# Optimization experiments

Measured on AMD Instinct MI355X. Metric: run time of the kernel, lower is better.

Reference implementation:

```python
import jax, jax.numpy as jnp
import numpy as np

B, T, S, PD = 512, 2048, 16, 4

def setup_inputs() -> dict:
    key = jax.random.key(0)
    ks = jax.random.split(key, 10)
    w = lambda k, sh: (jax.random.normal(k, sh, dtype=jnp.float32) * 0.1)
    return {
        'z': jax.random.normal(ks[0], (B, T, S), dtype=jnp.float32),
        'p': jax.random.normal(ks[1], (B, T, PD), dtype=jnp.float32),
        'mu0': jnp.zeros((B, S), dtype=jnp.float32),
        'P0': jnp.full((B, S), 0.1, dtype=jnp.float32),  # cfg['kf_P0']
        'Wq1': w(ks[2], (PD, 64)), 'bq1': jnp.zeros((64,), jnp.float32),
        'Wq2': w(ks[3], (64, S)),  'bq2': jnp.zeros((S,), jnp.float32),
        'Wr1': w(ks[4], (PD, 64)), 'br1': jnp.zeros((64,), jnp.float32),
        'Wr2': w(ks[5], (64, S)),  'br2': jnp.zeros((S,), jnp.float32),
        'Wg1': w(ks[6], (PD, 32)), 'bg1': jnp.zeros((32,), jnp.float32),
        'Wg2': w(ks[7], (32, 1)),  'bg2': jnp.zeros((1,), jnp.float32),
    }

def _mlp(x, W1, b1, W2, b2):
    return jax.nn.relu(x @ W1 + b1) @ W2 + b2

def reference(z, p, mu0, P0, Wq1, bq1, Wq2, bq2, Wr1, br1, Wr2, br2, Wg1, bg1, Wg2, bg2):
    # z: [B,T,S], p: [B,T,PD]; scan over time with batched Kalman state.
    zT = jnp.swapaxes(z, 0, 1)  # [T,B,S]
    pT = jnp.swapaxes(p, 0, 1)  # [T,B,PD]

    def step(carry, inp):
        mu, P = carry            # [B,S], [B,S]
        z_t, p_t = inp           # [B,S], [B,PD]
        Q_t = jax.nn.softplus(_mlp(p_t, Wq1, bq1, Wq2, bq2)) + 1e-8
        R_t = jax.nn.softplus(_mlp(p_t, Wr1, br1, Wr2, br2)) + 1e-8
        P_pred = P + Q_t
        K = jnp.clip(P_pred / (P_pred + R_t), 1e-6, 0.95)
        gamma_t = jax.nn.sigmoid(_mlp(p_t, Wg1, bg1, Wg2, bg2))  # [B,1] (scalar per sample)
        mu_new = mu + gamma_t * (K * (z_t - mu))
        P_new = (1.0 - K) * P_pred
        return (mu_new, P_new), mu_new

    (mu_f, P_f), mus = jax.lax.scan(step, (mu0, P0), (zT, pT))
    return jnp.swapaxes(mus, 0, 1)  # [B,T,S]
```

## Files before the change

kernel.cpp:

```cpp
#include <hip/hip_runtime.h>
#include <hip/hip_fp16.h>
#include <stdint.h>
#include <math.h>

#define KB 512
#define KT 2048
#define KS 16
#define KPD 4
#define QT 512
#define NQ (KT / QT)
#define QSTR 515
#define HSTR 40

typedef _Float16 f16;
typedef _Float16 f16x8 __attribute__((ext_vector_type(8)));
typedef float f32x4 __attribute__((ext_vector_type(4)));

#define MFMA16(A, B, C) __builtin_amdgcn_mfma_f32_16x16x32_f16(A, B, C, 0, 0, 0)

__device__ __forceinline__ float softplus_f(float x) {
    float ax = fabsf(x);
    float e  = __expf(-ax);
    return fmaxf(x, 0.0f) + __logf(1.0f + e);
}
__device__ __forceinline__ float sigmoid_f(float x) {
    return __builtin_amdgcn_rcpf(1.0f + __expf(-x));
}
__device__ __forceinline__ float h2f_lo(uint32_t w) {
    return __half2float(__ushort_as_half((unsigned short)(w & 0xffffu)));
}
__device__ __forceinline__ float h2f_hi(uint32_t w) {
    return __half2float(__ushort_as_half((unsigned short)(w >> 16)));
}
__device__ __forceinline__ f16x8 zero8() {
    f16x8 v;
#pragma unroll
    for (int i = 0; i < 8; ++i) v[i] = (f16)0;
    return v;
}
__device__ __forceinline__ int spos(int t) { return t ^ ((t >> 5) & 31); }

__device__ __forceinline__ uint32_t pkrelu(float a, float b) {
    auto h = __builtin_amdgcn_cvt_pkrtz(fmaxf(a, 0.f), fmaxf(b, 0.f));
    uint32_t w; __builtin_memcpy(&w, &h, 4);
    return w;
}
__device__ __forceinline__ uint16_t f2h(float x) {
    return (uint16_t)__half_as_ushort(__float2half_rn(x));
}
__device__ __forceinline__ float h2f(uint16_t x) {
    return __half2float(__ushort_as_half((unsigned short)x));
}

__global__ __launch_bounds__(512, 2) void kalman_ilp(
    const float* __restrict__ z, const float* __restrict__ p,
    const float* __restrict__ mu0, const float* __restrict__ P0,
    const float* __restrict__ Wq1, const float* __restrict__ bq1,
    const float* __restrict__ Wq2, const float* __restrict__ bq2,
    const float* __restrict__ Wr1, const float* __restrict__ br1,
    const float* __restrict__ Wr2, const float* __restrict__ br2,
    const float* __restrict__ Wg1, const float* __restrict__ bg1,
    const float* __restrict__ Wg2, const float* __restrict__ bg2,
    float* __restrict__ out)
{
    __shared__ __align__(16) uint32_t QRl[KS * QSTR];
    __shared__ __align__(16) float    Gl[QT];
    __shared__ __align__(16) uint16_t Hs[8 * KS * HSTR];
    __shared__ __align__(16) uint16_t zsh[KS * QSTR];

    const int tid = threadIdx.x;
    const int wv = tid >> 6;
    const int l = tid & 63;
    const int g = l >> 4;
    const int c = l & 15;
    const int b = blockIdx.x;

    f16* __restrict__ Hw = reinterpret_cast<f16*>(Hs) + wv * (KS * HSTR);

    const float* __restrict__ zb = z + (size_t)b * KT * KS;
    const float* __restrict__ pb = p + (size_t)b * KT * KPD;
    float* __restrict__ ob = out + (size_t)b * KT * KS;

    f16x8 fA1[10];
#pragma unroll
    for (int m = 0; m < 10; ++m) {
        const float* W = (m < 4) ? (Wq1 + m * 16)
                       : (m < 8) ? (Wr1 + (m - 4) * 16)
                                 : (Wg1 + (m - 8) * 16);
        const int ld = (m < 8) ? 64 : 32;
        float w0 = W[0 * ld + c], w1 = W[1 * ld + c],
              w2 = W[2 * ld + c], w3 = W[3 * ld + c];
        f16x8 a = zero8();
        if (g == 0) { a[0] = (f16)w0; a[1] = (f16)w1; a[2] = (f16)w2; a[3] = (f16)w3; }
        fA1[m] = a;
    }
    f16x8 fA2[5];
#pragma unroll
    for (int i = 0; i < 4; ++i) {
        const float* W = (i < 2) ? Wq2 : Wr2;
        const int kb = (i & 1) * 32;
        f16x8 a;
#pragma unroll
        for (int j = 0; j < 8; ++j) a[j] = (f16)W[(kb + g * 8 + j) * 16 + c];
        fA2[i] = a;
    }
    {
        f16x8 a = zero8();
        if (c == 0) {
#pragma unroll
            for (int j = 0; j < 8; ++j) a[j] = (f16)Wg2[g * 8 + j];
        }
        fA2[4] = a;
    }
    const float bQ0 = bq2[g * 4 + 0], bQ1 = bq2[g * 4 + 1],
                bQ2 = bq2[g * 4 + 2], bQ3 = bq2[g * 4 + 3];
    const float bR0 = br2[g * 4 + 0], bR1 = br2[g * 4 + 1],
                bR2 = br2[g * 4 + 2], bR3 = br2[g * 4 + 3];
    const float bG = bg2[0];

    float muA = mu0[b * KS + wv],     PA = P0[b * KS + wv];
    float muB = mu0[b * KS + wv + 8], PB = P0[b * KS + wv + 8];

    auto scan2 = [&](int sA, int sB, float& muqA, float& PqA, float& muqB, float& PqB) {
        uint32_t qrA[8], qrB[8];
        float zvA[8], zvB[8], gv[8];
        const uint32_t* qrowA = QRl + (size_t)sA * QSTR;
        const uint32_t* qrowB = QRl + (size_t)sB * QSTR;
#pragma unroll
        for (int i = 0; i < 8; ++i) {
            const int ps = spos(l * 8 + i);
            qrA[i] = qrowA[ps];
            qrB[i] = qrowB[ps];
            zvA[i] = h2f(zsh[sA * QSTR + ps]);
            zvB[i] = h2f(zsh[sB * QSTR + ps]);
            gv[i] = Gl[ps];
        }
        float a00 = 1.f, a01 = 0.f, a10 = 0.f, a11 = 1.f;
        float b00 = 1.f, b01 = 0.f, b10 = 0.f, b11 = 1.f;
#pragma unroll
        for (int i = 0; i < 8; ++i) {
            float QA = h2f_lo(qrA[i]), RA = h2f_hi(qrA[i]);
            float QB = h2f_lo(qrB[i]), RB = h2f_hi(qrB[i]);
            float taA = fmaf(QA, a10, a00), tbA = fmaf(QA, a11, a01);
            float taB = fmaf(QB, b10, b00), tbB = fmaf(QB, b11, b01);
            float n10A = fmaf(QA + RA, a10, a00), n11A = fmaf(QA + RA, a11, a01);
            float n10B = fmaf(QB + RB, b10, b00), n11B = fmaf(QB + RB, b11, b01);
            a00 = RA * taA; a01 = RA * tbA; a10 = n10A; a11 = n11A;
            b00 = RB * taB; b01 = RB * tbB; b10 = n10B; b11 = n11B;
        }
        float rnA = __builtin_amdgcn_rcpf(a11);
        float rnB = __builtin_amdgcn_rcpf(b11);
        float maA = a00 * rnA, mbA = a01 * rnA, mcA = a10 * rnA;
        float maB = b00 * rnB, mbB = b01 * rnB, mcB = b10 * rnB;
#pragma unroll
        for (int r = 0; r < 6; ++r) {
            const int d = 1 << r;
            float paA = __shfl_up(maA, d), pbA = __shfl_up(mbA, d), pcA = __shfl_up(mcA, d);
            float paB = __shfl_up(maB, d), pbB = __shfl_up(mbB, d), pcB = __shfl_up(mcB, d);
            float naA = fmaf(maA, paA, mbA * pcA);
            float naB = fmaf(maB, paB, mbB * pcB);
            float nbA = fmaf(maA, pbA, mbA);
            float nbB = fmaf(maB, pbB, mbB);
            float ncA = fmaf(mcA, paA, pcA);
            float ncB = fmaf(mcB, paB, pcB);
            float ndA = fmaf(mcA, pbA, 1.f);
            float ndB = fmaf(mcB, pbB, 1.f);
            float rrA = __builtin_amdgcn_rcpf(ndA);
            float rrB = __builtin_amdgcn_rcpf(ndB);
            bool act = (l >= d);
            maA = act ? naA * rrA : maA;  mbA = act ? nbA * rrA : mbA;  mcA = act ? ncA * rrA : mcA;
            maB = act ? naB * rrB : maB;  mbB = act ? nbB * rrB : mbB;  mcB = act ? ncB * rrB : mcB;
        }
        float eaA = __shfl_up(maA, 1), ebA = __shfl_up(mbA, 1), ecA = __shfl_up(mcA, 1);
        float eaB = __shfl_up(maB, 1), ebB = __shfl_up(mbB, 1), ecB = __shfl_up(mcB, 1);
        if (l == 0) { eaA = 1.f; ebA = 0.f; ecA = 0.f; eaB = 1.f; ebB = 0.f; ecB = 0.f; }
        float Pa = fmaf(eaA, PqA, ebA) * __builtin_amdgcn_rcpf(fmaf(ecA, PqA, 1.f));
        float Pb = fmaf(eaB, PqB, ebB) * __builtin_amdgcn_rcpf(fmaf(ecB, PqB, 1.f));

        float avA[8], bwA[8], avB[8], bwB[8];
        float AA = 1.f, BA = 0.f, AB = 1.f, BB = 0.f;
#pragma unroll
        for (int i = 0; i < 8; ++i) {
            float QA = h2f_lo(qrA[i]), RA = h2f_hi(qrA[i]);
            float QB = h2f_lo(qrB[i]), RB = h2f_hi(qrB[i]);
            float PpA = Pa + QA;
            float PpB = Pb + QB;
            float K0A = PpA * __builtin_amdgcn_rcpf(PpA + RA);
            float K0B = PpB * __builtin_amdgcn_rcpf(PpB + RB);
            float KkA = __builtin_amdgcn_fmed3f(K0A, 1e-6f, 0.95f);
            float KkB = __builtin_amdgcn_fmed3f(K0B, 1e-6f, 0.95f);
            float gkA = gv[i] * KkA;
            float gkB = gv[i] * KkB;
            avA[i] = 1.f - gkA;  bwA[i] = gkA * zvA[i];
            avB[i] = 1.f - gkB;  bwB[i] = gkB * zvB[i];
            Pa = fmaf(-KkA, PpA, PpA);
            Pb = fmaf(-KkB, PpB, PpB);
            AA = AA * avA[i];  BA = fmaf(avA[i], BA, bwA[i]);
            AB = AB * avB[i];  BB = fmaf(avB[i], BB, bwB[i]);
        }
        float PendA = __shfl(Pa, 63);
        float PendB = __shfl(Pb, 63);
#pragma unroll
        for (int r = 0; r < 6; ++r) {
            const int d = 1 << r;
            float pAA = __shfl_up(AA, d), pBA = __shfl_up(BA, d);
            float pAB = __shfl_up(AB, d), pBB = __shfl_up(BB, d);
            float nAA = AA * pAA;
            float nAB = AB * pAB;
            float nBA = fmaf(AA, pBA, BA);
            float nBB = fmaf(AB, pBB, BB);
            bool act = (l >= d);
            AA = act ? nAA : AA;  BA = act ? nBA : BA;
            AB = act ? nAB : AB;  BB = act ? nBB : BB;
        }
        float eAA = __shfl_up(AA, 1), eBA = __shfl_up(BA, 1);
        float eAB = __shfl_up(AB, 1), eBB = __shfl_up(BB, 1);
        if (l == 0) { eAA = 1.f; eBA = 0.f; eAB = 1.f; eBB = 0.f; }
        float muA_ = fmaf(eAA, muqA, eBA);
        float muB_ = fmaf(eAB, muqB, eBB);
#pragma unroll
        for (int i = 0; i < 8; ++i) {
            muA_ = fmaf(avA[i], muA_, bwA[i]);
            muB_ = fmaf(avB[i], muB_, bwB[i]);
            const int ps = spos(l * 8 + i);
            zsh[sA * QSTR + ps] = f2h(muA_);
            zsh[sB * QSTR + ps] = f2h(muB_);
        }
        muqA = __shfl(muA_, 63);
        muqB = __shfl(muB_, 63);
        PqA = PendA;
        PqB = PendB;
    };

    for (int q = 0; q < NQ; ++q) {
        {
            const int trow = q * QT + wv * 64;
            const float4 pv = *reinterpret_cast<const float4*>(pb + (size_t)(trow + l) * KPD);

#pragma unroll
            for (int n = 0; n < 4; ++n) {
                f16x8 fBP;
                {
                    const int src = n * 16 + c;
                    float x = __shfl(pv.x, src);
                    float y = __shfl(pv.y, src);
                    float zz = __shfl(pv.z, src);
                    float w = __shfl(pv.w, src);
                    fBP = zero8();
                    if (g == 0) { fBP[0] = (f16)x; fBP[1] = (f16)y; fBP[2] = (f16)zz; fBP[3] = (f16)w; }
                }

                f32x4 aq; aq[0] = bQ0; aq[1] = bQ1; aq[2] = bQ2; aq[3] = bQ3;
                f32x4 ar; ar[0] = bR0; ar[1] = bR1; ar[2] = bR2; ar[3] = bR3;
                f32x4 ag; ag[0] = 0.f; ag[1] = 0.f; ag[2] = 0.f; ag[3] = 0.f;

                uint32_t* Hd = reinterpret_cast<uint32_t*>(Hw);

#pragma unroll
                for (int X = 0; X < 5; ++X) {
                    const int m0 = 2 * X, m1 = 2 * X + 1;
                    {
                        const float* bs = (m0 < 4) ? (bq1 + m0 * 16)
                                        : (m0 < 8) ? (br1 + (m0 - 4) * 16)
                                                   : (bg1 + (m0 - 8) * 16);
                        f32x4 acc;
                        acc[0] = bs[g * 4 + 0]; acc[1] = bs[g * 4 + 1];
                        acc[2] = bs[g * 4 + 2]; acc[3] = bs[g * 4 + 3];
                        acc = MFMA16(fA1[m0], fBP, acc);
                        Hd[c * 20 + g * 2 + 0] = pkrelu(acc[0], acc[1]);
                        Hd[c * 20 + g * 2 + 1] = pkrelu(acc[2], acc[3]);
                    }
                    {
                        const float* bs = (m1 < 4) ? (bq1 + m1 * 16)
                                        : (m1 < 8) ? (br1 + (m1 - 4) * 16)
                                                   : (bg1 + (m1 - 8) * 16);
                        f32x4 acc;
                        acc[0] = bs[g * 4 + 0]; acc[1] = bs[g * 4 + 1];
                        acc[2] = bs[g * 4 + 2]; acc[3] = bs[g * 4 + 3];
                        acc = MFMA16(fA1[m1], fBP, acc);
                        Hd[c * 20 + 8 + g * 2 + 0] = pkrelu(acc[0], acc[1]);
                        Hd[c * 20 + 8 + g * 2 + 1] = pkrelu(acc[2], acc[3]);
                    }
                    f16x8 fb = *reinterpret_cast<const f16x8*>(Hw + c * HSTR + g * 8);
                    if (X == 0)      aq = MFMA16(fA2[0], fb, aq);
                    else if (X == 1) aq = MFMA16(fA2[1], fb, aq);
                    else if (X == 2) ar = MFMA16(fA2[2], fb, ar);
                    else if (X == 3) ar = MFMA16(fA2[3], fb, ar);
                    else             ag = MFMA16(fA2[4], fb, ag);
                }

                const int tt = wv * 64 + n * 16 + c;
                const int ps = spos(tt);
#pragma unroll
                for (int i = 0; i < 4; ++i) {
                    float Qv = softplus_f(aq[i]) + 1e-8f;
                    float Rv = softplus_f(ar[i]) + 1e-8f;
                    auto pk = __builtin_amdgcn_cvt_pkrtz(Qv, Rv);
                    uint32_t w; __builtin_memcpy(&w, &pk, 4);
                    QRl[(size_t)(g * 4 + i) * QSTR + ps] = w;
                }
                if (g == 0)
                    Gl[ps] = sigmoid_f(ag[0] + bG);
            }

            const float4* zq = reinterpret_cast<const float4*>(zb + (size_t)q * QT * KS);
#pragma unroll
            for (int v = 0; v < 4; ++v) {
                int k = tid + 512 * v;
                float4 w = zq[k];
                int t = k >> 2, s0 = (k & 3) << 2;
                const int ps = spos(t);
                zsh[(s0 + 0) * QSTR + ps] = f2h(w.x);
                zsh[(s0 + 1) * QSTR + ps] = f2h(w.y);
                zsh[(s0 + 2) * QSTR + ps] = f2h(w.z);
                zsh[(s0 + 3) * QSTR + ps] = f2h(w.w);
            }
        }
        __syncthreads();

        scan2(wv, wv + 8, muA, PA, muB, PB);
        __syncthreads();

        {
            float* od = ob + (size_t)q * QT * KS;
#pragma unroll
            for (int v = 0; v < 4; ++v) {
                int k = tid + 512 * v;
                int t = k >> 2, s0 = (k & 3) << 2;
                const int ps = spos(t);
                float4 w;
                w.x = h2f(zsh[(s0 + 0) * QSTR + ps]);
                w.y = h2f(zsh[(s0 + 1) * QSTR + ps]);
                w.z = h2f(zsh[(s0 + 2) * QSTR + ps]);
                w.w = h2f(zsh[(s0 + 3) * QSTR + ps]);
                *reinterpret_cast<float4*>(od + 4 * (size_t)k) = w;
            }
        }
        __syncthreads();
    }
}

__global__ __launch_bounds__(512, 2) void kalman_one(
    const float* __restrict__ z, const float* __restrict__ p,
    const float* __restrict__ mu0, const float* __restrict__ P0,
    const float* __restrict__ Wq1, const float* __restrict__ bq1,
    const float* __restrict__ Wq2, const float* __restrict__ bq2,
    const float* __restrict__ Wr1, const float* __restrict__ br1,
    const float* __restrict__ Wr2, const float* __restrict__ br2,
    const float* __restrict__ Wg1, const float* __restrict__ bg1,
    const float* __restrict__ Wg2, const float* __restrict__ bg2,
    float* __restrict__ out)
{
    __shared__ __align__(16) uint32_t QRl[KS * QSTR];
    __shared__ __align__(16) float    Gl[QT];
    __shared__ __align__(16) uint16_t Hs[8 * KS * HSTR];
    __shared__ __align__(16) uint16_t zsh[KS * QSTR];

    const int tid = threadIdx.x;
    const int wv = tid >> 6;
    const int l = tid & 63;
    const int g = l >> 4;
    const int c = l & 15;
    const int b = blockIdx.x;

    f16* __restrict__ Hw = reinterpret_cast<f16*>(Hs) + wv * (KS * HSTR);

    const float* __restrict__ zb = z + (size_t)b * KT * KS;
    const float* __restrict__ pb = p + (size_t)b * KT * KPD;
    float* __restrict__ ob = out + (size_t)b * KT * KS;

    f16x8 fA1[10];
#pragma unroll
    for (int m = 0; m < 10; ++m) {
        const float* W = (m < 4) ? (Wq1 + m * 16)
                       : (m < 8) ? (Wr1 + (m - 4) * 16)
                                 : (Wg1 + (m - 8) * 16);
        const int ld = (m < 8) ? 64 : 32;
        float w0 = W[0 * ld + c], w1 = W[1 * ld + c],
              w2 = W[2 * ld + c], w3 = W[3 * ld + c];
        f16x8 a = zero8();
        if (g == 0) { a[0] = (f16)w0; a[1] = (f16)w1; a[2] = (f16)w2; a[3] = (f16)w3; }
        fA1[m] = a;
    }
    f16x8 fA2[5];
#pragma unroll
    for (int i = 0; i < 4; ++i) {
        const float* W = (i < 2) ? Wq2 : Wr2;
        const int kb = (i & 1) * 32;
        f16x8 a;
#pragma unroll
        for (int j = 0; j < 8; ++j) a[j] = (f16)W[(kb + g * 8 + j) * 16 + c];
        fA2[i] = a;
    }
    {
        f16x8 a = zero8();
        if (c == 0) {
#pragma unroll
            for (int j = 0; j < 8; ++j) a[j] = (f16)Wg2[g * 8 + j];
        }
        fA2[4] = a;
    }
    const float bQ0 = bq2[g * 4 + 0], bQ1 = bq2[g * 4 + 1],
                bQ2 = bq2[g * 4 + 2], bQ3 = bq2[g * 4 + 3];
    const float bR0 = br2[g * 4 + 0], bR1 = br2[g * 4 + 1],
                bR2 = br2[g * 4 + 2], bR3 = br2[g * 4 + 3];
    const float bG = bg2[0];

    float muA = mu0[b * KS + wv],     PA = P0[b * KS + wv];
    float muB = mu0[b * KS + wv + 8], PB = P0[b * KS + wv + 8];

    auto scan_s = [&](int s, float& mu_q, float& P_q) {
        uint32_t qr[8];
        const uint32_t* qrow = QRl + (size_t)s * QSTR;
        float zvv[8], gvv[8];
#pragma unroll
        for (int i = 0; i < 8; ++i) {
            const int ps = spos(l * 8 + i);
            qr[i] = qrow[ps];
            zvv[i] = h2f(zsh[s * QSTR + ps]);
            gvv[i] = Gl[ps];
        }
        float c00 = 1.f, c01 = 0.f, c10 = 0.f, c11 = 1.f;
#pragma unroll
        for (int i = 0; i < 8; ++i) {
            float Q = h2f_lo(qr[i]), Rr = h2f_hi(qr[i]);
            float ta = fmaf(Q, c10, c00);
            float tb = fmaf(Q, c11, c01);
            float n10 = fmaf(Q + Rr, c10, c00);
            float n11 = fmaf(Q + Rr, c11, c01);
            c00 = Rr * ta; c01 = Rr * tb; c10 = n10; c11 = n11;
        }
        float rn = __builtin_amdgcn_rcpf(c11);
        float ma = c00 * rn, mb = c01 * rn, mc = c10 * rn;
#pragma unroll
        for (int r = 0; r < 6; ++r) {
            const int d = 1 << r;
            float pa = __shfl_up(ma, d);
            float pbv = __shfl_up(mb, d);
            float pc = __shfl_up(mc, d);
            float na = fmaf(ma, pa, mb * pc);
            float nb = fmaf(ma, pbv, mb);
            float nc = fmaf(mc, pa, pc);
            float nd = fmaf(mc, pbv, 1.f);
            float rr = __builtin_amdgcn_rcpf(nd);
            bool act = (l >= d);
            ma = act ? na * rr : ma;
            mb = act ? nb * rr : mb;
            mc = act ? nc * rr : mc;
        }
        float ea = __shfl_up(ma, 1);
        float eb = __shfl_up(mb, 1);
        float ec = __shfl_up(mc, 1);
        if (l == 0) { ea = 1.f; eb = 0.f; ec = 0.f; }
        float P = fmaf(ea, P_q, eb) * __builtin_amdgcn_rcpf(fmaf(ec, P_q, 1.f));

        float av[8], bw[8];
        float A = 1.f, Bv = 0.f;
#pragma unroll
        for (int i = 0; i < 8; ++i) {
            float Q = h2f_lo(qr[i]), Rr = h2f_hi(qr[i]);
            float Pp = P + Q;
            float K0 = Pp * __builtin_amdgcn_rcpf(Pp + Rr);
            float Kk = __builtin_amdgcn_fmed3f(K0, 1e-6f, 0.95f);
            float gk = gvv[i] * Kk;
            av[i] = 1.f - gk;
            bw[i] = gk * zvv[i];
            P = fmaf(-Kk, Pp, Pp);
            A = A * av[i];
            Bv = fmaf(av[i], Bv, bw[i]);
        }
        float P_end = __shfl(P, 63);
#pragma unroll
        for (int r = 0; r < 6; ++r) {
            const int d = 1 << r;
            float pA = __shfl_up(A, d);
            float pB = __shfl_up(Bv, d);
            float nA = A * pA;
            float nB = fmaf(A, pB, Bv);
            bool act = (l >= d);
            A  = act ? nA : A;
            Bv = act ? nB : Bv;
        }
        float eA = __shfl_up(A, 1);
        float eB = __shfl_up(Bv, 1);
        if (l == 0) { eA = 1.f; eB = 0.f; }
        float mu = fmaf(eA, mu_q, eB);
#pragma unroll
        for (int i = 0; i < 8; ++i) {
            mu = fmaf(av[i], mu, bw[i]);
            zsh[s * QSTR + spos(l * 8 + i)] = f2h(mu);
        }
        mu_q = __shfl(mu, 63);
        P_q = P_end;
    };

    for (int q = 0; q < NQ; ++q) {
        {
            const int trow = q * QT + wv * 64;
            const float4 pv = *reinterpret_cast<const float4*>(pb + (size_t)(trow + l) * KPD);

#pragma unroll
            for (int n = 0; n < 4; ++n) {
                f16x8 fBP;
                {
                    const int src = n * 16 + c;
                    float x = __shfl(pv.x, src);
                    float y = __shfl(pv.y, src);
                    float zz = __shfl(pv.z, src);
                    float w = __shfl(pv.w, src);
                    fBP = zero8();
                    if (g == 0) { fBP[0] = (f16)x; fBP[1] = (f16)y; fBP[2] = (f16)zz; fBP[3] = (f16)w; }
                }

                f32x4 aq; aq[0] = bQ0; aq[1] = bQ1; aq[2] = bQ2; aq[3] = bQ3;
                f32x4 ar; ar[0] = bR0; ar[1] = bR1; ar[2] = bR2; ar[3] = bR3;
                f32x4 ag; ag[0] = 0.f; ag[1] = 0.f; ag[2] = 0.f; ag[3] = 0.f;

                uint32_t* Hd = reinterpret_cast<uint32_t*>(Hw);

#pragma unroll
                for (int X = 0; X < 5; ++X) {
                    const int m0 = 2 * X, m1 = 2 * X + 1;
                    {
                        const float* bs = (m0 < 4) ? (bq1 + m0 * 16)
                                        : (m0 < 8) ? (br1 + (m0 - 4) * 16)
                                                   : (bg1 + (m0 - 8) * 16);
                        f32x4 acc;
                        acc[0] = bs[g * 4 + 0]; acc[1] = bs[g * 4 + 1];
                        acc[2] = bs[g * 4 + 2]; acc[3] = bs[g * 4 + 3];
                        acc = MFMA16(fA1[m0], fBP, acc);
                        Hd[c * 20 + g * 2 + 0] = pkrelu(acc[0], acc[1]);
                        Hd[c * 20 + g * 2 + 1] = pkrelu(acc[2], acc[3]);
                    }
                    {
                        const float* bs = (m1 < 4) ? (bq1 + m1 * 16)
                                        : (m1 < 8) ? (br1 + (m1 - 4) * 16)
                                                   : (bg1 + (m1 - 8) * 16);
                        f32x4 acc;
                        acc[0] = bs[g * 4 + 0]; acc[1] = bs[g * 4 + 1];
                        acc[2] = bs[g * 4 + 2]; acc[3] = bs[g * 4 + 3];
                        acc = MFMA16(fA1[m1], fBP, acc);
                        Hd[c * 20 + 8 + g * 2 + 0] = pkrelu(acc[0], acc[1]);
                        Hd[c * 20 + 8 + g * 2 + 1] = pkrelu(acc[2], acc[3]);
                    }
                    f16x8 fb = *reinterpret_cast<const f16x8*>(Hw + c * HSTR + g * 8);
                    if (X == 0)      aq = MFMA16(fA2[0], fb, aq);
                    else if (X == 1) aq = MFMA16(fA2[1], fb, aq);
                    else if (X == 2) ar = MFMA16(fA2[2], fb, ar);
                    else if (X == 3) ar = MFMA16(fA2[3], fb, ar);
                    else             ag = MFMA16(fA2[4], fb, ag);
                }

                const int tt = wv * 64 + n * 16 + c;
                const int ps = spos(tt);
#pragma unroll
                for (int i = 0; i < 4; ++i) {
                    float Qv = softplus_f(aq[i]) + 1e-8f;
                    float Rv = softplus_f(ar[i]) + 1e-8f;
                    auto pk = __builtin_amdgcn_cvt_pkrtz(Qv, Rv);
                    uint32_t w; __builtin_memcpy(&w, &pk, 4);
                    QRl[(size_t)(g * 4 + i) * QSTR + ps] = w;
                }
                if (g == 0)
                    Gl[ps] = sigmoid_f(ag[0] + bG);
            }

            const float4* zq = reinterpret_cast<const float4*>(zb + (size_t)q * QT * KS);
#pragma unroll
            for (int v = 0; v < 4; ++v) {
                int k = tid + 512 * v;
                float4 w = zq[k];
                int t = k >> 2, s0 = (k & 3) << 2;
                const int ps = spos(t);
                zsh[(s0 + 0) * QSTR + ps] = f2h(w.x);
                zsh[(s0 + 1) * QSTR + ps] = f2h(w.y);
                zsh[(s0 + 2) * QSTR + ps] = f2h(w.z);
                zsh[(s0 + 3) * QSTR + ps] = f2h(w.w);
            }
        }
        __syncthreads();

        scan_s(wv, muA, PA);
        scan_s(wv + 8, muB, PB);
        __syncthreads();

        {
            float* od = ob + (size_t)q * QT * KS;
#pragma unroll
            for (int v = 0; v < 4; ++v) {
                int k = tid + 512 * v;
                int t = k >> 2, s0 = (k & 3) << 2;
                const int ps = spos(t);
                float4 w;
                w.x = h2f(zsh[(s0 + 0) * QSTR + ps]);
                w.y = h2f(zsh[(s0 + 1) * QSTR + ps]);
                w.z = h2f(zsh[(s0 + 2) * QSTR + ps]);
                w.w = h2f(zsh[(s0 + 3) * QSTR + ps]);
                *reinterpret_cast<float4*>(od + 4 * (size_t)k) = w;
            }
        }
        __syncthreads();
    }
}

extern "C" void kernel_launch(void* const* d_in, const int* in_sizes, int n_in,
                              void* d_out, int out_size, void* d_ws, size_t ws_size,
                              hipStream_t stream) {
    const float* z   = (const float*)d_in[0];
    const float* p   = (const float*)d_in[1];
    const float* mu0 = (const float*)d_in[2];
    const float* P0  = (const float*)d_in[3];
    const float* Wq1 = (const float*)d_in[4];
    const float* bq1 = (const float*)d_in[5];
    const float* Wq2 = (const float*)d_in[6];
    const float* bq2 = (const float*)d_in[7];
    const float* Wr1 = (const float*)d_in[8];
    const float* br1 = (const float*)d_in[9];
    const float* Wr2 = (const float*)d_in[10];
    const float* br2 = (const float*)d_in[11];
    const float* Wg1 = (const float*)d_in[12];
    const float* bg1 = (const float*)d_in[13];
    const float* Wg2 = (const float*)d_in[14];
    const float* bg2 = (const float*)d_in[15];
    float* out = (float*)d_out;

    hipFuncAttributes attr{};
    bool use_ilp = false;
    if (hipFuncGetAttributes(&attr, (const void*)kalman_ilp) == hipSuccess)
        use_ilp = (attr.localSizeBytes <= 16);

    if (use_ilp) {
        hipLaunchKernelGGL(kalman_ilp, dim3(KB), dim3(512), 0, stream,
                           z, p, mu0, P0, Wq1, bq1, Wq2, bq2,
                           Wr1, br1, Wr2, br2, Wg1, bg1, Wg2, bg2, out);
    } else {
        hipLaunchKernelGGL(kalman_one, dim3(KB), dim3(512), 0, stream,
                           z, p, mu0, P0, Wq1, bq1, Wq2, bq2,
                           Wr1, br1, Wr2, br2, Wg1, bg1, Wg2, bg2, out);
    }
}
```

Baseline: 86.89 us.

## Shrink Kalman block to 256 threads with 256-step chunks and four states per wave

Replaces the 512-thread kernel with a 256-thread variant that processes time in 256-step chunks. Each wave now scans four state channels through two scan2 calls, and each lane handles 4 timesteps instead of 8. Shared memory per block shrinks, so more blocks can be resident at once. The cost is a longer serial chain per wave, twice as many chunk iterations with their syncs, and more shuffle-based prefix rounds relative to the sequential work per lane.

```diff
diff --git a/kernel.cpp b/kernel.cpp
--- a/kernel.cpp
+++ b/kernel.cpp
@@ -7,6 +7,9 @@
 #define KT 2048
 #define KS 16
 #define KPD 4
+#define ET 256
+#define NE (KT / ET)
+#define ESTR 259
 #define QT 512
 #define NQ (KT / QT)
 #define QSTR 515
@@ -52,7 +55,7 @@
     return __half2float(__ushort_as_half((unsigned short)x));
 }
 
-__global__ __launch_bounds__(512, 2) void kalman_ilp(
+__global__ __launch_bounds__(256, 2) void kalman_small(
     const float* __restrict__ z, const float* __restrict__ p,
     const float* __restrict__ mu0, const float* __restrict__ P0,
     const float* __restrict__ Wq1, const float* __restrict__ bq1,
@@ -63,10 +66,10 @@
     const float* __restrict__ Wg2, const float* __restrict__ bg2,
     float* __restrict__ out)
 {
-    __shared__ __align__(16) uint32_t QRl[KS * QSTR];
-    __shared__ __align__(16) float    Gl[QT];
-    __shared__ __align__(16) uint16_t Hs[8 * KS * HSTR];
-    __shared__ __align__(16) uint16_t zsh[KS * QSTR];
+    __shared__ __align__(16) uint32_t QRl[KS * ESTR];
+    __shared__ __align__(16) float    Gl[ET];
+    __shared__ __align__(16) uint16_t Hs[4 * KS * HSTR];
+    __shared__ __align__(16) uint16_t zsh[KS * ESTR];
 
     const int tid = threadIdx.x;
     const int wv = tid >> 6;
@@ -118,27 +121,29 @@
                 bR2 = br2[g * 4 + 2], bR3 = br2[g * 4 + 3];
     const float bG = bg2[0];
 
-    float muA = mu0[b * KS + wv],     PA = P0[b * KS + wv];
-    float muB = mu0[b * KS + wv + 8], PB = P0[b * KS + wv + 8];
+    float muA = mu0[b * KS + wv + 0],  PA = P0[b * KS + wv + 0];
+    float muB = mu0[b * KS + wv + 4],  PB = P0[b * KS + wv + 4];
+    float muC = mu0[b * KS + wv + 8],  PC = P0[b * KS + wv + 8];
+    float muD = mu0[b * KS + wv + 12], PD = P0[b * KS + wv + 12];
 
     auto scan2 = [&](int sA, int sB, float& muqA, float& PqA, float& muqB, float& PqB) {
-        uint32_t qrA[8], qrB[8];
-        float zvA[8], zvB[8], gv[8];
-        const uint32_t* qrowA = QRl + (size_t)sA * QSTR;
-        const uint32_t* qrowB = QRl + (size_t)sB * QSTR;
-#pragma unroll
-        for (int i = 0; i < 8; ++i) {
-            const int ps = spos(l * 8 + i);
+        uint32_t qrA[4], qrB[4];
+        float zvA[4], zvB[4], gv[4];
+        const uint32_t* qrowA = QRl + (size_t)sA * ESTR;
+        const uint32_t* qrowB = QRl + (size_t)sB * ESTR;
+#pragma unroll
+        for (int i = 0; i < 4; ++i) {
+            const int ps = spos(l * 4 + i);
             qrA[i] = qrowA[ps];
             qrB[i] = qrowB[ps];
-            zvA[i] = h2f(zsh[sA * QSTR + ps]);
-            zvB[i] = h2f(zsh[sB * QSTR + ps]);
+            zvA[i] = h2f(zsh[sA * ESTR + ps]);
+            zvB[i] = h2f(zsh[sB * ESTR + ps]);
             gv[i] = Gl[ps];
         }
         float a00 = 1.f, a01 = 0.f, a10 = 0.f, a11 = 1.f;
         float b00 = 1.f, b01 = 0.f, b10 = 0.f, b11 = 1.f;
 #pragma unroll
-        for (int i = 0; i < 8; ++i) {
+        for (int i = 0; i < 4; ++i) {
             float QA = h2f_lo(qrA[i]), RA = h2f_hi(qrA[i]);
             float QB = h2f_lo(qrB[i]), RB = h2f_hi(qrB[i]);
             float taA = fmaf(QA, a10, a00), tbA = fmaf(QA, a11, a01);
@@ -177,10 +182,10 @@
         float Pa = fmaf(eaA, PqA, ebA) * __builtin_amdgcn_rcpf(fmaf(ecA, PqA, 1.f));
         float Pb = fmaf(eaB, PqB, ebB) * __builtin_amdgcn_rcpf(fmaf(ecB, PqB, 1.f));
 
-        float avA[8], bwA[8], avB[8], bwB[8];
+        float avA[4], bwA[4], avB[4], bwB[4];
         float AA = 1.f, BA = 0.f, AB = 1.f, BB = 0.f;
 #pragma unroll
-        for (int i = 0; i < 8; ++i) {
+        for (int i = 0; i < 4; ++i) {
             float QA = h2f_lo(qrA[i]), RA = h2f_hi(qrA[i]);
             float QB = h2f_lo(qrB[i]), RB = h2f_hi(qrB[i]);
             float PpA = Pa + QA;
@@ -219,12 +224,12 @@
         float muA_ = fmaf(eAA, muqA, eBA);
         float muB_ = fmaf(eAB, muqB, eBB);
 #pragma unroll
-        for (int i = 0; i < 8; ++i) {
+        for (int i = 0; i < 4; ++i) {
             muA_ = fmaf(avA[i], muA_, bwA[i]);
             muB_ = fmaf(avB[i], muB_, bwB[i]);
-            const int ps = spos(l * 8 + i);
-            zsh[sA * QSTR + ps] = f2h(muA_);
-            zsh[sB * QSTR + ps] = f2h(muB_);
+            const int ps = spos(l * 4 + i);
+            zsh[sA * ESTR + ps] = f2h(muA_);
+            zsh[sB * ESTR + ps] = f2h(muB_);
         }
         muqA = __shfl(muA_, 63);
         muqB = __shfl(muB_, 63);
@@ -232,9 +237,9 @@
         PqB = PendB;
     };
 
-    for (int q = 0; q < NQ; ++q) {
+    for (int q = 0; q < NE; ++q) {
         {
-            const int trow = q * QT + wv * 64;
+            const int trow = q * ET + wv * 64;
             const float4 pv = *reinterpret_cast<const float4*>(pb + (size_t)(trow + l) * KPD);
 
 #pragma unroll
@@ -297,42 +302,43 @@
                     float Rv = softplus_f(ar[i]) + 1e-8f;
                     auto pk = __builtin_amdgcn_cvt_pkrtz(Qv, Rv);
                     uint32_t w; __builtin_memcpy(&w, &pk, 4);
-                    QRl[(size_t)(g * 4 + i) * QSTR + ps] = w;
+                    QRl[(size_t)(g * 4 + i) * ESTR + ps] = w;
                 }
                 if (g == 0)
                     Gl[ps] = sigmoid_f(ag[0] + bG);
             }
 
-            const float4* zq = reinterpret_cast<const float4*>(zb + (size_t)q * QT * KS);
+            const float4* zq = reinterpret_cast<const float4*>(zb + (size_t)q * ET * KS);
 #pragma unroll
             for (int v = 0; v < 4; ++v) {
-                int k = tid + 512 * v;
+                int k = tid + 256 * v;
                 float4 w = zq[k];
                 int t = k >> 2, s0 = (k & 3) << 2;
                 const int ps = spos(t);
-                zsh[(s0 + 0) * QSTR + ps] = f2h(w.x);
-                zsh[(s0 + 1) * QSTR + ps] = f2h(w.y);
-                zsh[(s0 + 2) * QSTR + ps] = f2h(w.z);
-                zsh[(s0 + 3) * QSTR + ps] = f2h(w.w);
+                zsh[(s0 + 0) * ESTR + ps] = f2h(w.x);
+                zsh[(s0 + 1) * ESTR + ps] = f2h(w.y);
+                zsh[(s0 + 2) * ESTR + ps] = f2h(w.z);
+                zsh[(s0 + 3) * ESTR + ps] = f2h(w.w);
             }
         }
         __syncthreads();
 
-        scan2(wv, wv + 8, muA, PA, muB, PB);
+        scan2(wv, wv + 4, muA, PA, muB, PB);
+        scan2(wv + 8, wv + 12, muC, PC, muD, PD);
         __syncthreads();
 
         {
-            float* od = ob + (size_t)q * QT * KS;
+            float* od = ob + (size_t)q * ET * KS;
 #pragma unroll
             for (int v = 0; v < 4; ++v) {
-                int k = tid + 512 * v;
+                int k = tid + 256 * v;
                 int t = k >> 2, s0 = (k & 3) << 2;
                 const int ps = spos(t);
                 float4 w;
-                w.x = h2f(zsh[(s0 + 0) * QSTR + ps]);
-                w.y = h2f(zsh[(s0 + 1) * QSTR + ps]);
-                w.z = h2f(zsh[(s0 + 2) * QSTR + ps]);
-                w.w = h2f(zsh[(s0 + 3) * QSTR + ps]);
+                w.x = h2f(zsh[(s0 + 0) * ESTR + ps]);
+                w.y = h2f(zsh[(s0 + 1) * ESTR + ps]);
+                w.z = h2f(zsh[(s0 + 2) * ESTR + ps]);
+                w.w = h2f(zsh[(s0 + 3) * ESTR + ps]);
                 *reinterpret_cast<float4*>(od + 4 * (size_t)k) = w;
             }
         }
@@ -625,12 +631,12 @@
     float* out = (float*)d_out;
 
     hipFuncAttributes attr{};
-    bool use_ilp = false;
-    if (hipFuncGetAttributes(&attr, (const void*)kalman_ilp) == hipSuccess)
-        use_ilp = (attr.localSizeBytes <= 16);
-
-    if (use_ilp) {
-        hipLaunchKernelGGL(kalman_ilp, dim3(KB), dim3(512), 0, stream,
+    bool use_small = false;
+    if (hipFuncGetAttributes(&attr, (const void*)kalman_small) == hipSuccess)
+        use_small = (attr.localSizeBytes <= 16);
+
+    if (use_small) {
+        hipLaunchKernelGGL(kalman_small, dim3(KB), dim3(256), 0, stream,
                            z, p, mu0, P0, Wq1, bq1, Wq2, bq2,
                            Wr1, br1, Wr2, br2, Wg1, bg1, Wg2, bg2, out);
     } else {
```

Result: slower. 92.28 us (+6.2%).
